# Performance work log

Hardware: AMD Instinct MI355X
Metric: run time of the kernel (lower is better)

## Reference

```python
import jax, jax.numpy as jnp
import numpy as np

B, T, D, H, K, V = 2, 2048, 2048, 16, 128, 128


def _l2norm(x, eps=1e-12):
    # F.normalize(p=2, dim=-1)
    n = jnp.sqrt(jnp.sum(x * x, axis=-1, keepdims=True))
    return x / jnp.maximum(n, eps)


def setup_inputs() -> dict:
    key = jax.random.key(0)
    ks = jax.random.split(key, 7)
    s = D ** -0.5
    return {
        "x": jax.random.normal(ks[0], (B, T, D), jnp.float32),
        "Wq": jax.random.normal(ks[1], (H * K, D), jnp.float32) * s,
        "Wk": jax.random.normal(ks[2], (H * K, D), jnp.float32) * s,
        "Wv": jax.random.normal(ks[3], (H * V, D), jnp.float32) * s,
        "Wa": jax.random.normal(ks[4], (H, D), jnp.float32) * s,
        "ba": jnp.zeros((H,), jnp.float32),
        "Wb": jax.random.normal(ks[5], (H, D), jnp.float32) * s,
        "bb": jnp.zeros((H,), jnp.float32),
    }


def _forward(x, Wq, Wk, Wv, Wa, ba, Wb, bb):
    Bq, Tq, _ = x.shape
    # projections (nn.Linear: y = x @ W.T)
    q = _l2norm(jnp.einsum('btd,od->bto', x, Wq).reshape(Bq, Tq, H, K))
    k = _l2norm(jnp.einsum('btd,od->bto', x, Wk).reshape(Bq, Tq, H, K))
    v = jnp.einsum('btd,od->bto', x, Wv).reshape(Bq, Tq, H, V)
    alpha = jax.nn.sigmoid(jnp.einsum('btd,hd->bth', x, Wa) + ba)          # [B,T,H] decay in (0,1)
    beta = jax.nn.softplus(jnp.einsum('btd,hd->bth', x, Wb) + bb) * K ** (-0.5)

    # gated delta rule recurrence over time (vectorized over B,H):
    #   S_t = a_t * S_{t-1} (I - b_t k_t k_t^T) + b_t v_t k_t^T ;  o_t = S_t q_t
    def step(S, inp):
        q_t, k_t, v_t, a_t, b_t = inp  # [B,H,K],[B,H,K],[B,H,V],[B,H],[B,H]
        Sd = S * a_t[..., None, None]                              # decay  [B,H,V,K]
        pred = jnp.einsum('bhvk,bhk->bhv', Sd, k_t)                # S k
        u = b_t[..., None] * (v_t - pred)                          # delta update [B,H,V]
        S_new = Sd + u[..., None] * k_t[:, :, None, :]             # rank-1 write
        o_t = jnp.einsum('bhvk,bhk->bhv', S_new, q_t)
        return S_new, o_t

    S0 = jnp.zeros((Bq, H, V, K), x.dtype)
    xs = (q.transpose(1, 0, 2, 3), k.transpose(1, 0, 2, 3),
          v.transpose(1, 0, 2, 3), alpha.transpose(1, 0, 2), beta.transpose(1, 0, 2))
    _, o = jax.lax.scan(step, S0, xs)
    return o.transpose(1, 0, 2, 3)  # [B,T,H,V]


def reference(x, Wq, Wk, Wv, Wa, ba, Wb, bb):
    return _forward(x, Wq, Wk, Wv, Wa, ba, Wb, bb)
```

## Files before the change

### kernel.cpp

```cpp
#include <hip/hip_runtime.h>
#include <math.h>

#define BB 2
#define TT 2048
#define DD 2048
#define HH 16
#define KK 128

typedef _Float16 h4 __attribute__((ext_vector_type(4)));
typedef _Float16 v8h __attribute__((ext_vector_type(8)));
typedef float v4f __attribute__((ext_vector_type(4)));

__global__ __launch_bounds__(256) void gemm_nt3(const float* __restrict__ A,
                                                const float* __restrict__ W0,
                                                const float* __restrict__ W1,
                                                const float* __restrict__ W2,
                                                float* __restrict__ Cbase,
                                                int M, int N, int Kd) {
  __shared__ float As[8][128];
  __shared__ float Bs[8][128];
  const int z = blockIdx.z;
  const float* W = (z == 0) ? W0 : (z == 1) ? W1 : W2;
  float* C = Cbase + (size_t)z * M * N;
  const int tid = threadIdx.x;
  const int bm = blockIdx.y * 128;
  const int bn = blockIdx.x * 128;
  const int lrow = tid >> 1;
  const int lcol = (tid & 1) * 4;
  const int rm = (tid >> 4) * 8;
  const int rn = (tid & 15) * 8;
  const float* Ap = A + (size_t)(bm + lrow) * Kd + lcol;
  const float* Wp = W + (size_t)(bn + lrow) * Kd + lcol;
  float acc[8][8];
#pragma unroll
  for (int i = 0; i < 8; i++)
#pragma unroll
    for (int j = 0; j < 8; j++) acc[i][j] = 0.f;
  float4 av = *(const float4*)Ap;
  float4 wv = *(const float4*)Wp;
  for (int d0 = 0; d0 < Kd; d0 += 8) {
    __syncthreads();
    As[lcol + 0][lrow] = av.x; As[lcol + 1][lrow] = av.y;
    As[lcol + 2][lrow] = av.z; As[lcol + 3][lrow] = av.w;
    Bs[lcol + 0][lrow] = wv.x; Bs[lcol + 1][lrow] = wv.y;
    Bs[lcol + 2][lrow] = wv.z; Bs[lcol + 3][lrow] = wv.w;
    __syncthreads();
    if (d0 + 8 < Kd) {
      av = *(const float4*)(Ap + d0 + 8);
      wv = *(const float4*)(Wp + d0 + 8);
    }
#pragma unroll
    for (int kk = 0; kk < 8; kk++) {
      const float4 a0 = *(const float4*)&As[kk][rm];
      const float4 a1 = *(const float4*)&As[kk][rm + 4];
      const float4 b0 = *(const float4*)&Bs[kk][rn];
      const float4 b1 = *(const float4*)&Bs[kk][rn + 4];
      const float ar[8] = {a0.x, a0.y, a0.z, a0.w, a1.x, a1.y, a1.z, a1.w};
      const float br[8] = {b0.x, b0.y, b0.z, b0.w, b1.x, b1.y, b1.z, b1.w};
#pragma unroll
      for (int i = 0; i < 8; i++)
#pragma unroll
        for (int j = 0; j < 8; j++) acc[i][j] = fmaf(ar[i], br[j], acc[i][j]);
    }
  }
#pragma unroll
  for (int i = 0; i < 8; i++) {
    float* cp = C + (size_t)(bm + rm + i) * N + bn + rn;
    float4 c0 = {acc[i][0], acc[i][1], acc[i][2], acc[i][3]};
    float4 c1 = {acc[i][4], acc[i][5], acc[i][6], acc[i][7]};
    *(float4*)cp = c0;
    *(float4*)(cp + 4) = c1;
  }
}

__global__ __launch_bounds__(256) void convert_f16(
    const float* __restrict__ x, const float* __restrict__ Wq,
    const float* __restrict__ Wk, const float* __restrict__ Wv,
    _Float16* __restrict__ xh, _Float16* __restrict__ xl,
    _Float16* __restrict__ Wf) {
  const size_t N4X = (size_t)BB * TT * DD / 4;
  const size_t N4W = (size_t)(HH * KK) * DD / 4;
  const size_t i = (size_t)blockIdx.x * 256 + threadIdx.x;
  if (i < N4X) {
    const float4 v = ((const float4*)x)[i];
    h4 hi, lo;
    hi.x = (_Float16)v.x; hi.y = (_Float16)v.y;
    hi.z = (_Float16)v.z; hi.w = (_Float16)v.w;
    lo.x = (_Float16)(v.x - (float)hi.x);
    lo.y = (_Float16)(v.y - (float)hi.y);
    lo.z = (_Float16)(v.z - (float)hi.z);
    lo.w = (_Float16)(v.w - (float)hi.w);
    ((h4*)xh)[i] = hi;
    ((h4*)xl)[i] = lo;
  } else {
    const size_t j = i - N4X;
    const float* Ws = (j < N4W) ? Wq : (j < 2 * N4W) ? Wk : Wv;
    const size_t jj = (j < N4W) ? j : (j < 2 * N4W) ? (j - N4W) : (j - 2 * N4W);
    const float4 v = ((const float4*)Ws)[jj];
    h4 hi;
    hi.x = (_Float16)v.x; hi.y = (_Float16)v.y;
    hi.z = (_Float16)v.z; hi.w = (_Float16)v.w;
    ((h4*)Wf)[j] = hi;
  }
}

#define GLDS(gp, lp)                                              \
  __builtin_amdgcn_global_load_lds(                               \
      (const __attribute__((address_space(1))) void*)(gp),        \
      (__attribute__((address_space(3))) void*)(lp), 16, 0, 0)

__global__ __launch_bounds__(256) void gemm_mfma(
    const _Float16* __restrict__ xh, const _Float16* __restrict__ xl,
    const _Float16* __restrict__ Wf, float* __restrict__ Cbase) {
  __shared__ float4 lraw[1536];
  _Float16* Ah = (_Float16*)lraw;
  _Float16* Al = Ah + 4096;
  _Float16* Bs = Al + 4096;

  const int z = blockIdx.z;
  const _Float16* W = Wf + (size_t)z * DD * (HH * KK);
  float* C = Cbase + (size_t)z * (BB * TT) * (HH * KK);

  const int tid = threadIdx.x;
  const int w = tid >> 6;
  const int lane = tid & 63;
  const int bm = blockIdx.y * 128;
  const int bn = blockIdx.x * 128;
  const int wm = (w & 1) * 64;
  const int wn = (w >> 1) * 64;
  const int m16 = lane & 15;
  const int quad = lane >> 4;

  const _Float16* gAh = xh + (size_t)(bm + (tid >> 2)) * DD + (tid & 3) * 8;
  const _Float16* gAl = xl + (size_t)(bm + (tid >> 2)) * DD + (tid & 3) * 8;
  const _Float16* gB = W + (size_t)(bn + (tid >> 2)) * DD + (tid & 3) * 8;
  const int lb = w * 512;

  v4f acc[4][4];
#pragma unroll
  for (int i = 0; i < 4; i++)
#pragma unroll
    for (int j = 0; j < 4; j++) acc[i][j] = (v4f){0.f, 0.f, 0.f, 0.f};

  for (int d0 = 0; d0 < DD; d0 += 32) {
    GLDS(gAh + d0, Ah + lb);
    GLDS(gAh + d0 + 64 * DD, Ah + 2048 + lb);
    GLDS(gAl + d0, Al + lb);
    GLDS(gAl + d0 + 64 * DD, Al + 2048 + lb);
    GLDS(gB + d0, Bs + lb);
    GLDS(gB + d0 + 64 * DD, Bs + 2048 + lb);
    __syncthreads();
    v8h ah[4], al[4], bw[4];
#pragma unroll
    for (int i = 0; i < 4; i++) {
      ah[i] = *(const v8h*)&Ah[(wm + i * 16 + m16) * 32 + quad * 8];
      al[i] = *(const v8h*)&Al[(wm + i * 16 + m16) * 32 + quad * 8];
      bw[i] = *(const v8h*)&Bs[(wn + i * 16 + m16) * 32 + quad * 8];
    }
#pragma unroll
    for (int mi = 0; mi < 4; mi++)
#pragma unroll
      for (int ni = 0; ni < 4; ni++) {
        acc[mi][ni] = __builtin_amdgcn_mfma_f32_16x16x32_f16(ah[mi], bw[ni],
                                                             acc[mi][ni], 0, 0, 0);
        acc[mi][ni] = __builtin_amdgcn_mfma_f32_16x16x32_f16(al[mi], bw[ni],
                                                             acc[mi][ni], 0, 0, 0);
      }
    __syncthreads();
  }
#pragma unroll
  for (int mi = 0; mi < 4; mi++) {
#pragma unroll
    for (int r = 0; r < 4; r++) {
      float* cp =
          C + (size_t)(bm + wm + mi * 16 + quad * 4 + r) * (HH * KK) + bn + wn + m16;
#pragma unroll
      for (int ni = 0; ni < 4; ni++) cp[ni * 16] = acc[mi][ni][r];
    }
  }
}

__global__ __launch_bounds__(64) void ab_proj(const float* __restrict__ x,
                                              const float* __restrict__ Wa,
                                              const float* __restrict__ ba,
                                              const float* __restrict__ Wb,
                                              const float* __restrict__ bb,
                                              float* __restrict__ abq) {
  const int row = blockIdx.x;
  const int g = blockIdx.y;
  const int h0 = (g & 1) * 8;
  const bool isA = (g < 2);
  const float* W = isA ? Wa : Wb;
  const int lane = threadIdx.x;
  const float* xr = x + (size_t)row * DD;
  float acc[8];
#pragma unroll
  for (int j = 0; j < 8; j++) acc[j] = 0.f;
  for (int d = lane; d < DD; d += 64) {
    const float xv = xr[d];
#pragma unroll
    for (int j = 0; j < 8; j++)
      acc[j] = fmaf(xv, W[(size_t)(h0 + j) * DD + d], acc[j]);
  }
#pragma unroll
  for (int j = 0; j < 8; j++) {
#pragma unroll
    for (int off = 32; off > 0; off >>= 1) acc[j] += __shfl_xor(acc[j], off, 64);
  }
  if (lane == 0) {
    if (isA) {
#pragma unroll
      for (int j = 0; j < 8; j++) {
        const float z = acc[j] + ba[h0 + j];
        abq[((size_t)row * HH + h0 + j) * 4 + 0] = 1.0f / (1.0f + expf(-z));
      }
    } else {
#pragma unroll
      for (int j = 0; j < 8; j++) {
        const float z = acc[j] + bb[h0 + j];
        const float sp = (z > 20.f) ? z : log1pf(expf(z));
        abq[((size_t)row * HH + h0 + j) * 4 + 1] = sp * 0.08838834764831845f;
      }
    }
  }
}

__global__ __launch_bounds__(256) void norm_qk(float* __restrict__ q,
                                               float* __restrict__ k,
                                               float* __restrict__ abq) {
  const int vec = blockIdx.x * 4 + (threadIdx.x >> 6);
  const int l = threadIdx.x & 63;
  float* qp = q + (size_t)vec * 128;
  float* kp = k + (size_t)vec * 128;
  float q0 = qp[l], q1 = qp[l + 64];
  float k0 = kp[l], k1 = kp[l + 64];
  float sq = q0 * q0 + q1 * q1;
  float sk = k0 * k0 + k1 * k1;
#pragma unroll
  for (int off = 32; off > 0; off >>= 1) {
    sq += __shfl_xor(sq, off, 64);
    sk += __shfl_xor(sk, off, 64);
  }
  const float iq = 1.0f / fmaxf(sqrtf(sq), 1e-12f);
  const float ik = 1.0f / fmaxf(sqrtf(sk), 1e-12f);
  q0 *= iq; q1 *= iq; k0 *= ik; k1 *= ik;
  qp[l] = q0; qp[l + 64] = q1;
  kp[l] = k0; kp[l + 64] = k1;
  float pq = q0 * k0 + q1 * k1;
#pragma unroll
  for (int off = 32; off > 0; off >>= 1) pq += __shfl_xor(pq, off, 64);
  if (l == 0) abq[(size_t)vec * 4 + 2] = pq;
}

#define DPP_ADD(x, ctrl)                                                     \
  ((x) + __int_as_float(__builtin_amdgcn_update_dpp(                         \
             0, __float_as_int(x), (ctrl), 0xF, 0xF, true)))

#define SCAN_STEP(kc0, kc1, qc0, qc1, vc, ac, store_ptr)                       \
  {                                                                            \
    float dkA = fmaf(S0, kc0.x, fmaf(S1, kc0.y, fmaf(S2, kc0.z, S3 * kc0.w))); \
    float dkB = fmaf(S4, kc1.x, fmaf(S5, kc1.y, fmaf(S6, kc1.z, S7 * kc1.w))); \
    float dqA = fmaf(S0, qc0.x, fmaf(S1, qc0.y, fmaf(S2, qc0.z, S3 * qc0.w))); \
    float dqB = fmaf(S4, qc1.x, fmaf(S5, qc1.y, fmaf(S6, qc1.z, S7 * qc1.w))); \
    float dk = dkA + dkB;                                                      \
    float dq = dqA + dqB;                                                      \
    dk = DPP_ADD(dk, 0xB1);  dq = DPP_ADD(dq, 0xB1);             \
    dk = DPP_ADD(dk, 0x4E);  dq = DPP_ADD(dq, 0x4E);             \
    dk = DPP_ADD(dk, 0x141); dq = DPP_ADD(dq, 0x141);            \
    dk = DPP_ADD(dk, 0x140); dq = DPP_ADD(dq, 0x140);            \
    const float u = ac.y * (vc - ac.x * dk);                                   \
    const float oo = fmaf(ac.x, dq, u * ac.z);                                 \
    S0 = fmaf(ac.x, S0, u * kc0.x);                                            \
    S1 = fmaf(ac.x, S1, u * kc0.y);                                            \
    S2 = fmaf(ac.x, S2, u * kc0.z);                                            \
    S3 = fmaf(ac.x, S3, u * kc0.w);                                            \
    S4 = fmaf(ac.x, S4, u * kc1.x);                                            \
    S5 = fmaf(ac.x, S5, u * kc1.y);                                            \
    S6 = fmaf(ac.x, S6, u * kc1.z);                                            \
    S7 = fmaf(ac.x, S7, u * kc1.w);                                            \
    if (g == 0) *(store_ptr) = oo;                                             \
  }

#define PD 8

__global__ __launch_bounds__(256) void scan_kernel(const float* __restrict__ q,
                                                   const float* __restrict__ k,
                                                   const float* __restrict__ v,
                                                   const float* __restrict__ abq,
                                                   float* __restrict__ o) {
  const int bid = blockIdx.x;
  const int bh = bid & 31;
  const int s = bid >> 5;
  const int h = bh & 15;
  const int b = bh >> 4;
  const int tid = threadIdx.x;
  const int w = tid >> 6;
  const int lane = tid & 63;
  const int rg = lane >> 4;
  const int g = lane & 15;
  const int vrow = s * 16 + w * 4 + rg;

  const size_t base = (size_t)b * TT * 2048 + (size_t)h * KK;
  const float* kb = k + base + g * 8;
  const float* qb = q + base + g * 8;
  const float* vb = v + base + vrow;
  const float* ab = abq + ((size_t)b * TT * HH + h) * 4;
  float* ob = o + base + vrow;

  float S0 = 0.f, S1 = 0.f, S2 = 0.f, S3 = 0.f;
  float S4 = 0.f, S5 = 0.f, S6 = 0.f, S7 = 0.f;

  float4 kf0[PD], kf1[PD], qf0[PD], qf1[PD], af[PD];
  float vf[PD];
#pragma unroll
  for (int d = 0; d < PD; d++) {
    kf0[d] = *(const float4*)(kb + d * 2048);
    kf1[d] = *(const float4*)(kb + d * 2048 + 4);
    qf0[d] = *(const float4*)(qb + d * 2048);
    qf1[d] = *(const float4*)(qb + d * 2048 + 4);
    vf[d] = vb[d * 2048];
    af[d] = *(const float4*)(ab + d * 64);
  }

  int off = 0;
  int aoff = 0;
  for (int t0 = 0; t0 < TT - PD; t0 += PD) {
#pragma unroll
    for (int j = 0; j < PD; j++) {
      SCAN_STEP(kf0[j], kf1[j], qf0[j], qf1[j], vf[j], af[j],
                ob + off + j * 2048);
      kf0[j] = *(const float4*)(kb + off + (j + PD) * 2048);
      kf1[j] = *(const float4*)(kb + off + (j + PD) * 2048 + 4);
      qf0[j] = *(const float4*)(qb + off + (j + PD) * 2048);
      qf1[j] = *(const float4*)(qb + off + (j + PD) * 2048 + 4);
      vf[j] = vb[off + (j + PD) * 2048];
      af[j] = *(const float4*)(ab + aoff + (j + PD) * 64);
      __builtin_amdgcn_sched_barrier(0);
    }
    off += PD * 2048;
    aoff += PD * 64;
  }
#pragma unroll
  for (int j = 0; j < PD; j++) {
    SCAN_STEP(kf0[j], kf1[j], qf0[j], qf1[j], vf[j], af[j], ob + off + j * 2048);
  }
}

extern "C" void kernel_launch(void* const* d_in, const int* in_sizes, int n_in,
                              void* d_out, int out_size, void* d_ws,
                              size_t ws_size, hipStream_t stream) {
  const float* x = (const float*)d_in[0];
  const float* Wq = (const float*)d_in[1];
  const float* Wk = (const float*)d_in[2];
  const float* Wv = (const float*)d_in[3];
  const float* Wa = (const float*)d_in[4];
  const float* ba = (const float*)d_in[5];
  const float* Wb = (const float*)d_in[6];
  const float* bb = (const float*)d_in[7];
  float* out = (float*)d_out;
  float* ws = (float*)d_ws;

  const size_t PROJ = (size_t)BB * TT * HH * KK;
  const size_t NABQ = (size_t)BB * TT * HH * 4;
  float* qw = ws;
  float* kw = ws + PROJ;
  float* vw = ws + 2 * PROJ;
  float* abq = ws + 3 * PROJ;
  _Float16* xh = (_Float16*)(abq + NABQ);
  _Float16* xl = xh + (size_t)BB * TT * DD;
  _Float16* Wf = xl + (size_t)BB * TT * DD;
  const size_t NEED = (3 * PROJ + NABQ) * 4 +
                      ((size_t)BB * TT * DD * 2 + 3 * (size_t)(HH * KK) * DD) * 2;

  const int M = BB * TT;
  const int N = HH * KK;
  if (ws_size >= NEED) {
    const int cgrid = (int)(((size_t)BB * TT * DD / 4 + 3 * (size_t)N * DD / 4) / 256);
    convert_f16<<<cgrid, 256, 0, stream>>>(x, Wq, Wk, Wv, xh, xl, Wf);
    gemm_mfma<<<dim3(N / 128, M / 128, 3), 256, 0, stream>>>(xh, xl, Wf, qw);
  } else {
    gemm_nt3<<<dim3(N / 128, M / 128, 3), 256, 0, stream>>>(x, Wq, Wk, Wv, qw,
                                                            M, N, DD);
  }
  ab_proj<<<dim3(M, 4), 64, 0, stream>>>(x, Wa, ba, Wb, bb, abq);
  norm_qk<<<(BB * TT * HH) / 4, 256, 0, stream>>>(qw, kw, abq);
  scan_kernel<<<BB * HH * 8, 256, 0, stream>>>(qw, kw, vw, abq, out);
}
```

Before: 779.2 us.

## Pack normalized q/k as interleaved fp16 for the scan kernel

The normalization kernel now writes the L2-normalized k and q together in one interleaved half-precision buffer, one 256-element record per (b,t,h), instead of overwriting the fp32 arrays in place. The scan kernel reads one 16-byte vector each for k and q per step rather than four float4 loads, and converts to fp32 before the FMAs. This halves the q/k bytes the latency-bound recurrence streams and makes the per-step loads contiguous. The cost is fp16 rounding of q and k, which accumulates through the 2048-step state recurrence and may affect accuracy; the workspace region previously used for xh is reused as the fp16 buffer.

```diff
diff --git a/kernel.cpp b/kernel.cpp
--- a/kernel.cpp
+++ b/kernel.cpp
@@ -225,13 +225,14 @@
   }
 }
 
-__global__ __launch_bounds__(256) void norm_qk(float* __restrict__ q,
-                                               float* __restrict__ k,
-                                               float* __restrict__ abq) {
+__global__ __launch_bounds__(256) void norm_pack(const float* __restrict__ q,
+                                                 const float* __restrict__ k,
+                                                 _Float16* __restrict__ kq,
+                                                 float* __restrict__ abq) {
   const int vec = blockIdx.x * 4 + (threadIdx.x >> 6);
   const int l = threadIdx.x & 63;
-  float* qp = q + (size_t)vec * 128;
-  float* kp = k + (size_t)vec * 128;
+  const float* qp = q + (size_t)vec * 128;
+  const float* kp = k + (size_t)vec * 128;
   float q0 = qp[l], q1 = qp[l + 64];
   float k0 = kp[l], k1 = kp[l + 64];
   float sq = q0 * q0 + q1 * q1;
@@ -243,10 +244,14 @@
   }
   const float iq = 1.0f / fmaxf(sqrtf(sq), 1e-12f);
   const float ik = 1.0f / fmaxf(sqrtf(sk), 1e-12f);
-  q0 *= iq; q1 *= iq; k0 *= ik; k1 *= ik;
-  qp[l] = q0; qp[l + 64] = q1;
-  kp[l] = k0; kp[l + 64] = k1;
-  float pq = q0 * k0 + q1 * k1;
+  const _Float16 hq0 = (_Float16)(q0 * iq), hq1 = (_Float16)(q1 * iq);
+  const _Float16 hk0 = (_Float16)(k0 * ik), hk1 = (_Float16)(k1 * ik);
+  _Float16* kv = kq + (size_t)vec * 256;
+  kv[l] = hk0;
+  kv[l + 64] = hk1;
+  kv[l + 128] = hq0;
+  kv[l + 192] = hq1;
+  float pq = (float)hq0 * (float)hk0 + (float)hq1 * (float)hk1;
 #pragma unroll
   for (int off = 32; off > 0; off >>= 1) pq += __shfl_xor(pq, off, 64);
   if (l == 0) abq[(size_t)vec * 4 + 2] = pq;
@@ -256,12 +261,20 @@
   ((x) + __int_as_float(__builtin_amdgcn_update_dpp(                         \
              0, __float_as_int(x), (ctrl), 0xF, 0xF, true)))
 
-#define SCAN_STEP(kc0, kc1, qc0, qc1, vc, ac, store_ptr)                       \
+#define SCAN_STEP(kc, qc, vc, ac, store_ptr)                                   \
   {                                                                            \
-    float dkA = fmaf(S0, kc0.x, fmaf(S1, kc0.y, fmaf(S2, kc0.z, S3 * kc0.w))); \
-    float dkB = fmaf(S4, kc1.x, fmaf(S5, kc1.y, fmaf(S6, kc1.z, S7 * kc1.w))); \
-    float dqA = fmaf(S0, qc0.x, fmaf(S1, qc0.y, fmaf(S2, qc0.z, S3 * qc0.w))); \
-    float dqB = fmaf(S4, qc1.x, fmaf(S5, qc1.y, fmaf(S6, qc1.z, S7 * qc1.w))); \
+    float dkA = fmaf((float)kc[0], S0,                                         \
+                     fmaf((float)kc[1], S1,                                    \
+                          fmaf((float)kc[2], S2, (float)kc[3] * S3)));         \
+    float dkB = fmaf((float)kc[4], S4,                                         \
+                     fmaf((float)kc[5], S5,                                    \
+                          fmaf((float)kc[6], S6, (float)kc[7] * S7)));         \
+    float dqA = fmaf((float)qc[0], S0,                                         \
+                     fmaf((float)qc[1], S1,                                    \
+                          fmaf((float)qc[2], S2, (float)qc[3] * S3)));         \
+    float dqB = fmaf((float)qc[4], S4,                                         \
+                     fmaf((float)qc[5], S5,                                    \
+                          fmaf((float)qc[6], S6, (float)qc[7] * S7)));         \
     float dk = dkA + dkB;                                                      \
     float dq = dqA + dqB;                                                      \
     dk = DPP_ADD(dk, 0xB1);  dq = DPP_ADD(dq, 0xB1);             \
@@ -270,24 +283,23 @@
     dk = DPP_ADD(dk, 0x140); dq = DPP_ADD(dq, 0x140);            \
     const float u = ac.y * (vc - ac.x * dk);                                   \
     const float oo = fmaf(ac.x, dq, u * ac.z);                                 \
-    S0 = fmaf(ac.x, S0, u * kc0.x);                                            \
-    S1 = fmaf(ac.x, S1, u * kc0.y);                                            \
-    S2 = fmaf(ac.x, S2, u * kc0.z);                                            \
-    S3 = fmaf(ac.x, S3, u * kc0.w);                                            \
-    S4 = fmaf(ac.x, S4, u * kc1.x);                                            \
-    S5 = fmaf(ac.x, S5, u * kc1.y);                                            \
-    S6 = fmaf(ac.x, S6, u * kc1.z);                                            \
-    S7 = fmaf(ac.x, S7, u * kc1.w);                                            \
+    S0 = fmaf(ac.x, S0, u * (float)kc[0]);                                     \
+    S1 = fmaf(ac.x, S1, u * (float)kc[1]);                                     \
+    S2 = fmaf(ac.x, S2, u * (float)kc[2]);                                     \
+    S3 = fmaf(ac.x, S3, u * (float)kc[3]);                                     \
+    S4 = fmaf(ac.x, S4, u * (float)kc[4]);                                     \
+    S5 = fmaf(ac.x, S5, u * (float)kc[5]);                                     \
+    S6 = fmaf(ac.x, S6, u * (float)kc[6]);                                     \
+    S7 = fmaf(ac.x, S7, u * (float)kc[7]);                                     \
     if (g == 0) *(store_ptr) = oo;                                             \
   }
 
 #define PD 8
-
-__global__ __launch_bounds__(256) void scan_kernel(const float* __restrict__ q,
-                                                   const float* __restrict__ k,
-                                                   const float* __restrict__ v,
-                                                   const float* __restrict__ abq,
-                                                   float* __restrict__ o) {
+#define KQSTRIDE (HH * 256)
+
+__global__ __launch_bounds__(256) void scan_kernel(
+    const _Float16* __restrict__ kq, const float* __restrict__ v,
+    const float* __restrict__ abq, float* __restrict__ o) {
   const int bid = blockIdx.x;
   const int bh = bid & 31;
   const int s = bid >> 5;
@@ -300,49 +312,45 @@
   const int g = lane & 15;
   const int vrow = s * 16 + w * 4 + rg;
 
-  const size_t base = (size_t)b * TT * 2048 + (size_t)h * KK;
-  const float* kb = k + base + g * 8;
-  const float* qb = q + base + g * 8;
-  const float* vb = v + base + vrow;
+  const _Float16* kqb = kq + ((size_t)b * TT * HH + h) * 256 + g * 8;
+  const float* vb = v + (size_t)b * TT * 2048 + (size_t)h * KK + vrow;
   const float* ab = abq + ((size_t)b * TT * HH + h) * 4;
-  float* ob = o + base + vrow;
+  float* ob = o + (size_t)b * TT * 2048 + (size_t)h * KK + vrow;
 
   float S0 = 0.f, S1 = 0.f, S2 = 0.f, S3 = 0.f;
   float S4 = 0.f, S5 = 0.f, S6 = 0.f, S7 = 0.f;
 
-  float4 kf0[PD], kf1[PD], qf0[PD], qf1[PD], af[PD];
+  v8h kf[PD], qf[PD];
+  float4 af[PD];
   float vf[PD];
 #pragma unroll
   for (int d = 0; d < PD; d++) {
-    kf0[d] = *(const float4*)(kb + d * 2048);
-    kf1[d] = *(const float4*)(kb + d * 2048 + 4);
-    qf0[d] = *(const float4*)(qb + d * 2048);
-    qf1[d] = *(const float4*)(qb + d * 2048 + 4);
+    kf[d] = *(const v8h*)(kqb + d * KQSTRIDE);
+    qf[d] = *(const v8h*)(kqb + d * KQSTRIDE + 128);
     vf[d] = vb[d * 2048];
     af[d] = *(const float4*)(ab + d * 64);
   }
 
   int off = 0;
+  int offv = 0;
   int aoff = 0;
   for (int t0 = 0; t0 < TT - PD; t0 += PD) {
 #pragma unroll
     for (int j = 0; j < PD; j++) {
-      SCAN_STEP(kf0[j], kf1[j], qf0[j], qf1[j], vf[j], af[j],
-                ob + off + j * 2048);
-      kf0[j] = *(const float4*)(kb + off + (j + PD) * 2048);
-      kf1[j] = *(const float4*)(kb + off + (j + PD) * 2048 + 4);
-      qf0[j] = *(const float4*)(qb + off + (j + PD) * 2048);
-      qf1[j] = *(const float4*)(qb + off + (j + PD) * 2048 + 4);
-      vf[j] = vb[off + (j + PD) * 2048];
+      SCAN_STEP(kf[j], qf[j], vf[j], af[j], ob + offv + j * 2048);
+      kf[j] = *(const v8h*)(kqb + off + (j + PD) * KQSTRIDE);
+      qf[j] = *(const v8h*)(kqb + off + (j + PD) * KQSTRIDE + 128);
+      vf[j] = vb[offv + (j + PD) * 2048];
       af[j] = *(const float4*)(ab + aoff + (j + PD) * 64);
       __builtin_amdgcn_sched_barrier(0);
     }
-    off += PD * 2048;
+    off += PD * KQSTRIDE;
+    offv += PD * 2048;
     aoff += PD * 64;
   }
 #pragma unroll
   for (int j = 0; j < PD; j++) {
-    SCAN_STEP(kf0[j], kf1[j], qf0[j], qf1[j], vf[j], af[j], ob + off + j * 2048);
+    SCAN_STEP(kf[j], qf[j], vf[j], af[j], ob + offv + j * 2048);
   }
 }
 
@@ -374,15 +382,18 @@
 
   const int M = BB * TT;
   const int N = HH * KK;
+  _Float16* kqf16;
   if (ws_size >= NEED) {
     const int cgrid = (int)(((size_t)BB * TT * DD / 4 + 3 * (size_t)N * DD / 4) / 256);
     convert_f16<<<cgrid, 256, 0, stream>>>(x, Wq, Wk, Wv, xh, xl, Wf);
     gemm_mfma<<<dim3(N / 128, M / 128, 3), 256, 0, stream>>>(xh, xl, Wf, qw);
+    kqf16 = xh;
   } else {
     gemm_nt3<<<dim3(N / 128, M / 128, 3), 256, 0, stream>>>(x, Wq, Wk, Wv, qw,
                                                             M, N, DD);
+    kqf16 = (_Float16*)(abq + NABQ);
   }
   ab_proj<<<dim3(M, 4), 64, 0, stream>>>(x, Wa, ba, Wb, bb, abq);
-  norm_qk<<<(BB * TT * HH) / 4, 256, 0, stream>>>(qw, kw, abq);
-  scan_kernel<<<BB * HH * 8, 256, 0, stream>>>(qw, kw, vw, abq, out);
-}
+  norm_pack<<<(BB * TT * HH) / 4, 256, 0, stream>>>(qw, kw, kqf16, abq);
+  scan_kernel<<<BB * HH * 8, 256, 0, stream>>>(kqf16, vw, abq, out);
+}
```

Result: slower. 827.5 us (+6.2%).

## Stage scan inputs through LDS with async global-to-LDS loads and packed FMA

Applied to the files above, without the earlier changes.

The recurrence kernel now stages k, q, v and the per-step scalars for windows of 8 timesteps into a 4-slot LDS ring using global_load_lds, prefetching two windows ahead with waitcnt and barrier sync. It replaces per-thread strided global loads that each lane repeated. The state update and dot products use 2-wide packed FMA vectors. The cost is block-wide barriers per window and extra LDS reads per step. The hand-coded waitcnt values risk ordering mistakes.

```diff
diff --git a/kernel.cpp b/kernel.cpp
--- a/kernel.cpp
+++ b/kernel.cpp
@@ -10,6 +10,7 @@
 typedef _Float16 h4 __attribute__((ext_vector_type(4)));
 typedef _Float16 v8h __attribute__((ext_vector_type(8)));
 typedef float v4f __attribute__((ext_vector_type(4)));
+typedef float v2f __attribute__((ext_vector_type(2)));
 
 __global__ __launch_bounds__(256) void gemm_nt3(const float* __restrict__ A,
                                                 const float* __restrict__ W0,
@@ -108,6 +109,10 @@
   __builtin_amdgcn_global_load_lds(                               \
       (const __attribute__((address_space(1))) void*)(gp),        \
       (__attribute__((address_space(3))) void*)(lp), 16, 0, 0)
+#define GLDS4(gp, lp)                                             \
+  __builtin_amdgcn_global_load_lds(                               \
+      (const __attribute__((address_space(1))) void*)(gp),        \
+      (__attribute__((address_space(3))) void*)(lp), 4, 0, 0)
 
 __global__ __launch_bounds__(256) void gemm_mfma(
     const _Float16* __restrict__ xh, const _Float16* __restrict__ xl,
@@ -256,38 +261,23 @@
   ((x) + __int_as_float(__builtin_amdgcn_update_dpp(                         \
              0, __float_as_int(x), (ctrl), 0xF, 0xF, true)))
 
-#define SCAN_STEP(kc0, kc1, qc0, qc1, vc, ac, store_ptr)                       \
-  {                                                                            \
-    float dkA = fmaf(S0, kc0.x, fmaf(S1, kc0.y, fmaf(S2, kc0.z, S3 * kc0.w))); \
-    float dkB = fmaf(S4, kc1.x, fmaf(S5, kc1.y, fmaf(S6, kc1.z, S7 * kc1.w))); \
-    float dqA = fmaf(S0, qc0.x, fmaf(S1, qc0.y, fmaf(S2, qc0.z, S3 * qc0.w))); \
-    float dqB = fmaf(S4, qc1.x, fmaf(S5, qc1.y, fmaf(S6, qc1.z, S7 * qc1.w))); \
-    float dk = dkA + dkB;                                                      \
-    float dq = dqA + dqB;                                                      \
-    dk = DPP_ADD(dk, 0xB1);  dq = DPP_ADD(dq, 0xB1);             \
-    dk = DPP_ADD(dk, 0x4E);  dq = DPP_ADD(dq, 0x4E);             \
-    dk = DPP_ADD(dk, 0x141); dq = DPP_ADD(dq, 0x141);            \
-    dk = DPP_ADD(dk, 0x140); dq = DPP_ADD(dq, 0x140);            \
-    const float u = ac.y * (vc - ac.x * dk);                                   \
-    const float oo = fmaf(ac.x, dq, u * ac.z);                                 \
-    S0 = fmaf(ac.x, S0, u * kc0.x);                                            \
-    S1 = fmaf(ac.x, S1, u * kc0.y);                                            \
-    S2 = fmaf(ac.x, S2, u * kc0.z);                                            \
-    S3 = fmaf(ac.x, S3, u * kc0.w);                                            \
-    S4 = fmaf(ac.x, S4, u * kc1.x);                                            \
-    S5 = fmaf(ac.x, S5, u * kc1.y);                                            \
-    S6 = fmaf(ac.x, S6, u * kc1.z);                                            \
-    S7 = fmaf(ac.x, S7, u * kc1.w);                                            \
-    if (g == 0) *(store_ptr) = oo;                                             \
-  }
-
-#define PD 8
+#define WSTEPS 8
+#define NWIN (TT / WSTEPS)
+#define VB 32768
+#define ABB 34816
+#define V2F(p) (*(const v2f*)&(p))
+
+struct Slot {
+  float4 kA, kB, qA, qB, ab;
+  float vv;
+};
 
 __global__ __launch_bounds__(256) void scan_kernel(const float* __restrict__ q,
                                                    const float* __restrict__ k,
                                                    const float* __restrict__ v,
                                                    const float* __restrict__ abq,
                                                    float* __restrict__ o) {
+  __shared__ __attribute__((aligned(16))) char lds[35328];
   const int bid = blockIdx.x;
   const int bh = bid & 31;
   const int s = bid >> 5;
@@ -298,51 +288,113 @@
   const int lane = tid & 63;
   const int rg = lane >> 4;
   const int g = lane & 15;
-  const int vrow = s * 16 + w * 4 + rg;
-
-  const size_t base = (size_t)b * TT * 2048 + (size_t)h * KK;
-  const float* kb = k + base + g * 8;
-  const float* qb = q + base + g * 8;
-  const float* vb = v + base + vrow;
-  const float* ab = abq + ((size_t)b * TT * HH + h) * 4;
-  float* ob = o + base + vrow;
-
-  float S0 = 0.f, S1 = 0.f, S2 = 0.f, S3 = 0.f;
-  float S4 = 0.f, S5 = 0.f, S6 = 0.f, S7 = 0.f;
-
-  float4 kf0[PD], kf1[PD], qf0[PD], qf1[PD], af[PD];
-  float vf[PD];
-#pragma unroll
-  for (int d = 0; d < PD; d++) {
-    kf0[d] = *(const float4*)(kb + d * 2048);
-    kf1[d] = *(const float4*)(kb + d * 2048 + 4);
-    qf0[d] = *(const float4*)(qb + d * 2048);
-    qf1[d] = *(const float4*)(qb + d * 2048 + 4);
-    vf[d] = vb[d * 2048];
-    af[d] = *(const float4*)(ab + d * 64);
-  }
-
-  int off = 0;
-  int aoff = 0;
-  for (int t0 = 0; t0 < TT - PD; t0 += PD) {
-#pragma unroll
-    for (int j = 0; j < PD; j++) {
-      SCAN_STEP(kf0[j], kf1[j], qf0[j], qf1[j], vf[j], af[j],
-                ob + off + j * 2048);
-      kf0[j] = *(const float4*)(kb + off + (j + PD) * 2048);
-      kf1[j] = *(const float4*)(kb + off + (j + PD) * 2048 + 4);
-      qf0[j] = *(const float4*)(qb + off + (j + PD) * 2048);
-      qf1[j] = *(const float4*)(qb + off + (j + PD) * 2048 + 4);
-      vf[j] = vb[off + (j + PD) * 2048];
-      af[j] = *(const float4*)(ab + aoff + (j + PD) * 64);
+  const int rowloc = w * 4 + rg;
+  const int vrow = s * 16 + rowloc;
+
+  float* ob = o + (size_t)b * TT * 2048 + (size_t)h * KK + vrow;
+
+  auto stage = [&](int Wst) {
+    const int t0 = Wst * WSTEPS;
+    const int slot = Wst & 3;
+#pragma unroll
+    for (int i = 0; i < 3; i++) {
+      const int id = w * 3 + i;
+      if (id < 8) {
+        const int t = t0 + id;
+        const size_t vecbase = ((size_t)(b * TT + t) * HH + h) * 128;
+        const float* src = (lane < 32) ? (k + vecbase + lane * 4)
+                                       : (q + vecbase + (size_t)(lane - 32) * 4);
+        GLDS(src, lds + slot * 8192 + id * 1024);
+      } else if (id < 10) {
+        const int t4 = t0 + (id - 8) * 4;
+        const float* src = v + (size_t)(b * TT + t4 + (lane >> 4)) * 2048 +
+                           h * 128 + s * 16 + (lane & 15);
+        GLDS4(src, lds + VB + slot * 512 + (id - 8) * 256);
+      } else {
+        if (lane < 8) {
+          const float* src =
+              abq + ((size_t)(b * TT + t0 + lane) * HH + h) * 4;
+          GLDS(src, lds + ABB + slot * 128);
+        }
+      }
+    }
+  };
+
+#define LOAD_SLOT(S_, t_)                                                   \
+  {                                                                         \
+    const int _m = (t_) & 31;                                               \
+    S_.kA = *(const float4*)(lds + _m * 1024 + g * 32);                     \
+    S_.kB = *(const float4*)(lds + _m * 1024 + g * 32 + 16);                \
+    S_.qA = *(const float4*)(lds + _m * 1024 + 512 + g * 32);               \
+    S_.qB = *(const float4*)(lds + _m * 1024 + 512 + g * 32 + 16);          \
+    S_.vv = *(const float*)(lds + VB + _m * 64 + rowloc * 4);               \
+    S_.ab = *(const float4*)(lds + ABB + _m * 16);                          \
+  }
+
+#define STEP(S_, t_)                                                        \
+  {                                                                         \
+    const v2f k0 = V2F(S_.kA.x), k1 = V2F(S_.kA.z);                         \
+    const v2f k2 = V2F(S_.kB.x), k3 = V2F(S_.kB.z);                         \
+    const v2f q0 = V2F(S_.qA.x), q1 = V2F(S_.qA.z);                         \
+    const v2f q2 = V2F(S_.qB.x), q3 = V2F(S_.qB.z);                         \
+    v2f aK = __builtin_elementwise_fma(                                     \
+        k0, Sv0,                                                            \
+        __builtin_elementwise_fma(                                          \
+            k1, Sv1, __builtin_elementwise_fma(k2, Sv2, k3 * Sv3)));        \
+    v2f aQ = __builtin_elementwise_fma(                                     \
+        q0, Sv0,                                                            \
+        __builtin_elementwise_fma(                                          \
+            q1, Sv1, __builtin_elementwise_fma(q2, Sv2, q3 * Sv3)));        \
+    float dk = aK.x + aK.y, dq = aQ.x + aQ.y;                               \
+    dk = DPP_ADD(dk, 0xB1);  dq = DPP_ADD(dq, 0xB1);                        \
+    dk = DPP_ADD(dk, 0x4E);  dq = DPP_ADD(dq, 0x4E);                        \
+    dk = DPP_ADD(dk, 0x141); dq = DPP_ADD(dq, 0x141);                       \
+    dk = DPP_ADD(dk, 0x140); dq = DPP_ADD(dq, 0x140);                       \
+    const float a_ = S_.ab.x, b_ = S_.ab.y, kqd = S_.ab.z;                  \
+    const float u = b_ * (S_.vv - a_ * dk);                                 \
+    const float oo = fmaf(a_, dq, u * kqd);                                 \
+    const v2f a2 = {a_, a_}, u2 = {u, u};                                   \
+    Sv0 = __builtin_elementwise_fma(a2, Sv0, u2 * k0);                      \
+    Sv1 = __builtin_elementwise_fma(a2, Sv1, u2 * k1);                      \
+    Sv2 = __builtin_elementwise_fma(a2, Sv2, u2 * k2);                      \
+    Sv3 = __builtin_elementwise_fma(a2, Sv3, u2 * k3);                      \
+    if (g == 0) ob[(size_t)(t_) * 2048] = oo;                               \
+  }
+
+  stage(0);
+  stage(1);
+  __builtin_amdgcn_s_waitcnt(0x0F70);
+  __builtin_amdgcn_s_barrier();
+
+  Slot slA, slB;
+  LOAD_SLOT(slA, 0);
+  LOAD_SLOT(slB, 1);
+
+  v2f Sv0 = {0.f, 0.f}, Sv1 = {0.f, 0.f}, Sv2 = {0.f, 0.f}, Sv3 = {0.f, 0.f};
+
+  for (int W = 0; W < NWIN; W++) {
+    if (W >= 1) {
+      __builtin_amdgcn_s_waitcnt(0x0F78);
+      __builtin_amdgcn_s_barrier();
+    }
+    if (W + 2 < NWIN) stage(W + 2);
+    const int t0 = W * WSTEPS;
+#pragma unroll
+    for (int j = 0; j < WSTEPS; j += 2) {
+      const int t = t0 + j;
+      STEP(slA, t);
+      {
+        const int tp = (t + 2 < TT) ? t + 2 : t;
+        LOAD_SLOT(slA, tp);
+      }
       __builtin_amdgcn_sched_barrier(0);
-    }
-    off += PD * 2048;
-    aoff += PD * 64;
-  }
-#pragma unroll
-  for (int j = 0; j < PD; j++) {
-    SCAN_STEP(kf0[j], kf1[j], qf0[j], qf1[j], vf[j], af[j], ob + off + j * 2048);
+      STEP(slB, t + 1);
+      {
+        const int tp = (t + 3 < TT) ? t + 3 : t;
+        LOAD_SLOT(slB, tp);
+      }
+      __builtin_amdgcn_sched_barrier(0);
+    }
   }
 }
 
```

Result: slower. 814.8 us (+4.6%).
